# Kernel optimization log

Hardware: AMD Instinct MI355X
Metric: run time of the kernel (lower is better)

## Reference

```python
import jax, jax.numpy as jnp
import numpy as np

NUM_HEADS = 8
N_MOD = 3


def _sinusoidal_pe(seq_len, d_model):
    # standard sinusoidal table [seq_len, d_model]
    pos = np.arange(seq_len, dtype=np.float32)[:, None]
    div = np.exp(np.arange(0, d_model, 2, dtype=np.float32) * (-np.log(10000.0) / d_model))
    pe = np.zeros((seq_len, d_model), dtype=np.float32)
    pe[:, 0::2] = np.sin(pos * div)
    pe[:, 1::2] = np.cos(pos * div)
    return jnp.asarray(pe)


def _attn_mask(dim_x, dim_z, n_mod):
    # additive mask [dim_x, dim_x + n_mod*dim_z]: 0 where allowed, -inf elsewhere
    blocks = [np.eye(dim_x, dtype=np.float32)]
    for _ in range(n_mod):  # all modalities present (mod_list == full_mod)
        p2 = np.zeros((dim_x, dim_z), dtype=np.float32)
        p2[dim_x - dim_z:, :] = np.eye(dim_z, dtype=np.float32)
        blocks.append(p2)
    m = np.concatenate(blocks, axis=1)
    return jnp.asarray(np.where(m < 1, -np.inf, 0.0).astype(np.float32))


def setup_inputs() -> dict:
    key = jax.random.key(0)
    ks = jax.random.split(key, 8)
    bs, en, dx, dz = 32, 256, 512, 256
    state = jax.random.normal(ks[0], (bs, en, dx), jnp.float32)
    obs0 = jax.random.normal(ks[1], (bs, en, dz), jnp.float32)
    obs1 = jax.random.normal(ks[2], (bs, en, dz), jnp.float32)
    obs2 = jax.random.normal(ks[3], (bs, en, dz), jnp.float32)
    Q = jax.random.uniform(ks[4], (dx, en), jnp.float32)  # torch.rand init
    Wq = jax.random.normal(ks[5], (en, en), jnp.float32) / np.sqrt(en)
    Wk = jax.random.normal(ks[6], (en, en), jnp.float32) / np.sqrt(en)
    bq = jnp.zeros((en,), jnp.float32)
    bk = jnp.zeros((en,), jnp.float32)
    return {"state": state, "obs0": obs0, "obs1": obs1, "obs2": obs2,
            "Q": Q, "Wq": Wq, "bq": bq, "Wk": Wk, "bk": bk}


def reference(state, obs0, obs1, obs2, Q, Wq, bq, Wk, bk):
    bs, en, dx = state.shape
    dz = obs0.shape[2]
    obs_list = (obs0, obs1, obs2)
    mask = _attn_mask(dx, dz, N_MOD)            # [dx, L]
    pe = _sinusoidal_pe(bs, en)                 # positions run over batch axis (faithful quirk)

    # mean-center over the ensemble axis
    A = state - jnp.mean(state, axis=1, keepdims=True)          # [bs, en, dx]
    Ys = [o - jnp.mean(o, axis=1, keepdims=True) for o in obs_list]

    # build query / key-value sequences in [tokens, bs, en] layout, add PE, then batch-major
    q = Q[:, None, :] + pe[None, :, :]                          # [dx, bs, en]
    xy = jnp.concatenate([jnp.transpose(A, (2, 0, 1))]
                         + [jnp.transpose(Y, (2, 0, 1)) for Y in Ys], axis=0)
    xy = xy + pe[None, :, :]                                    # [L, bs, en]
    qb = jnp.transpose(q, (1, 0, 2))                            # [bs, dx, en]
    kb = jnp.transpose(xy, (1, 0, 2))                           # [bs, L, en]

    # multi-head masked attention (output path is discarded by the original module,
    # only the attention map is used, so no V/O projection is needed)
    dh = en // NUM_HEADS
    qh = (qb @ Wq + bq).reshape(bs, dx, NUM_HEADS, dh).transpose(0, 2, 1, 3)   # [bs,h,dx,dh]
    kh = (kb @ Wk + bk).reshape(bs, -1, NUM_HEADS, dh).transpose(0, 2, 1, 3)   # [bs,h,L,dh]
    scores = jnp.einsum('bhqd,bhkd->bhqk', qh, kh) / np.sqrt(dh).astype(np.float32)
    scores = scores + mask[None, None, :, :]
    atten = jnp.mean(jax.nn.softmax(scores, axis=-1), axis=1)   # [bs, dx, L]

    # attn-weighted matmul over concatenated raw state+obs
    merge = jnp.concatenate([state, obs0, obs1, obs2], axis=2)  # [bs, en, L]
    new_state = jnp.einsum('bql,bel->beq', atten, merge)        # [bs, en, dx]
    return new_state, atten
```

## Files before the change

### kernel.cpp

```cpp
#include <hip/hip_runtime.h>
#include <math.h>


__global__ __launch_bounds__(256)
void k_uv_copy(const float* __restrict__ Q, const float* __restrict__ Wq,
               const float* __restrict__ bq, const float* __restrict__ state,
               float* __restrict__ uT, float* __restrict__ vT,
               float* __restrict__ out0) {
  const int blk = blockIdx.x;
  const int t = threadIdx.x;
  if (blk < 288) {
    __shared__ float row[256];
    float rv;
    if (blk < 256) {
      rv = Q[(256 + blk) * 256 + t];
    } else {
      const int b = blk - 256;
      const float dv = expf(-9.210340371976184f * (float)((t >> 1) << 1) * (1.0f / 256.0f));
      const float ang = (float)b * dv;
      rv = (t & 1) ? cosf(ang) : sinf(ang);
    }
    row[t] = rv;
    __syncthreads();
    float acc = (blk < 256) ? 0.0f : bq[t];
    for (int e = 0; e < 256; ++e) acc += row[e] * Wq[e * 256 + t];
    if (blk < 256) uT[t * 256 + blk] = acc;
    else           vT[t * 32 + (blk - 256)] = acc;
  } else {
    const int id = blk - 288;
    const int b = id >> 5, eg = id & 31;
    const int r = t >> 5;
    const int c = t & 31;
    const int e = eg * 8 + r;
    const size_t base = ((size_t)(b * 256 + e)) * 512;
    *(float4*)(out0 + base + c * 4)        = *(const float4*)(state + base + c * 4);
    *(float4*)(out0 + base + (c + 32) * 4) = *(const float4*)(state + base + (c + 32) * 4);
  }
}

__global__ __launch_bounds__(256)
void k_w_onehot(const float* __restrict__ Wk, const float* __restrict__ uT,
                const float* __restrict__ vT, float* __restrict__ wu2,
                float* __restrict__ wv, float* __restrict__ out1) {
  const int blk = blockIdx.x;
  const int t = threadIdx.x;
  if (blk < 512) {
    const int e = blk & 255;
    const int part = blk >> 8;
    __shared__ float wrow[256];
    wrow[t] = Wk[e * 256 + t];
    __syncthreads();
    if (part == 0) {
#pragma unroll
      for (int h = 0; h < 8; ++h) {
        float acc = 0.0f;
#pragma unroll
        for (int d = 0; d < 32; ++d)
          acc += uT[(h * 32 + d) * 256 + t] * wrow[h * 32 + d];
        wu2[(h * 256 + e) * 256 + t] = acc;
      }
    } else if (t < 32) {
#pragma unroll
      for (int h = 0; h < 8; ++h) {
        float acc = 0.0f;
#pragma unroll
        for (int d = 0; d < 32; ++d)
          acc += vT[(h * 32 + d) * 32 + t] * wrow[h * 32 + d];
        wv[(t * 8 + h) * 256 + e] = acc;
      }
    }
  } else {
    const int id = blk - 512;
    const int b = id >> 5, qg = id & 31;
#pragma unroll
    for (int k = 0; k < 8; ++k) {
      const int q = qg * 8 + k;
      float4* row = (float4*)(out1 + ((size_t)(b * 512 + q)) * 1280);
      float4 o = make_float4(0.f, 0.f, 0.f, 0.f);
      if (t == (q >> 2)) {
        const int comp = q & 3;
        if (comp == 0) o.x = 1.f; else if (comp == 1) o.y = 1.f;
        else if (comp == 2) o.z = 1.f; else o.w = 1.f;
      }
      row[t] = o;
      if (t < 64) row[256 + t] = make_float4(0.f, 0.f, 0.f, 0.f);
    }
  }
}

__global__ __launch_bounds__(512)
void k_dot(const float* __restrict__ state, const float* __restrict__ o0,
           const float* __restrict__ o1, const float* __restrict__ o2,
           const float* __restrict__ wu2, const float* __restrict__ wv,
           float* __restrict__ pws) {
  const int t = threadIdx.x;
  const int jt = blockIdx.x;
  const int eq = blockIdx.y;
  const int b  = blockIdx.z;

  __shared__ float s_data[4][64][17];
  __shared__ float s_wv[512];
  __shared__ float s_part[8][16][25];

#pragma unroll
  for (int rep = 0; rep < 2; ++rep) {
    const int c = t + rep * 512;
    const int m = c >> 8;
    const int r = c & 255;
    const int e = r >> 2;
    const int jq = r & 3;
    const int ge = eq * 64 + e;
    const int j0 = jt * 16 + jq * 4;
    const float* src;
    if (m == 0)      src = state + ((size_t)(b * 256 + ge)) * 512 + 256 + j0;
    else if (m == 1) src = o0 + ((size_t)(b * 256 + ge)) * 256 + j0;
    else if (m == 2) src = o1 + ((size_t)(b * 256 + ge)) * 256 + j0;
    else             src = o2 + ((size_t)(b * 256 + ge)) * 256 + j0;
    const float4 v4 = *(const float4*)src;
    const int jb = jq * 4;
    s_data[m][e][jb]   = v4.x; s_data[m][e][jb+1] = v4.y;
    s_data[m][e][jb+2] = v4.z; s_data[m][e][jb+3] = v4.w;
  }
  s_wv[t & 511] = wv[b * 2048 + ((t & 511) >> 6) * 256 + eq * 64 + (t & 63)];
  __syncthreads();

  const int jl = t & 15;
  const int es = (t >> 4) & 15;
  const int hp = t >> 8;
  const int j = jt * 16 + jl;

  float acc[24];
#pragma unroll
  for (int k = 0; k < 24; ++k) acc[k] = 0.f;

  const float* pwu = wu2 + (size_t)hp * 4 * 256 * 256 + j;
  const float* pwv = s_wv + hp * 4 * 64;

#pragma unroll
  for (int it = 0; it < 4; ++it) {
    const int el = it * 16 + es;
    const int e = eq * 64 + el;
    const float s  = s_data[0][el][jl];
    const float x0 = s_data[1][el][jl];
    const float x1 = s_data[2][el][jl];
    const float x2 = s_data[3][el][jl];
    acc[20] += s; acc[21] += x0; acc[22] += x1; acc[23] += x2;
#pragma unroll
    for (int hh = 0; hh < 4; ++hh) {
      const float w = pwu[(size_t)(hh * 256 + e) * 256] + pwv[hh * 64 + el];
      acc[hh * 5 + 0] += s * w;  acc[hh * 5 + 1] += x0 * w;
      acc[hh * 5 + 2] += x1 * w; acc[hh * 5 + 3] += x2 * w;
      acc[hh * 5 + 4] += w;
    }
  }

#pragma unroll
  for (int k = 0; k < 24; ++k) {
    acc[k] += __shfl_xor(acc[k], 16);
    acc[k] += __shfl_xor(acc[k], 32);
  }
  if ((t & 48) == 0) {
    const int w = t >> 6;
    float* p = &s_part[w][jl][0];
#pragma unroll
    for (int k = 0; k < 24; ++k) p[k] = acc[k];
  }
  __syncthreads();

  const size_t base = (((size_t)(jt * 32 + b)) * 4 + eq) * 704;
  if (t < 16) {
#pragma unroll
    for (int k = 0; k < 20; ++k) {
      float s = s_part[0][t][k] + s_part[1][t][k] + s_part[2][t][k] + s_part[3][t][k];
      pws[base + k * 16 + t] = s;
    }
#pragma unroll
    for (int c = 0; c < 4; ++c) {
      float s = s_part[0][t][20 + c] + s_part[1][t][20 + c] +
                s_part[2][t][20 + c] + s_part[3][t][20 + c];
      pws[base + (40 + c) * 16 + t] = s;
    }
  } else if (t >= 256 && t < 272) {
    const int l = t & 15;
#pragma unroll
    for (int k = 0; k < 20; ++k) {
      float s = s_part[4][l][k] + s_part[5][l][k] + s_part[6][l][k] + s_part[7][l][k];
      pws[base + (20 + k) * 16 + l] = s;
    }
  }
}

__global__ __launch_bounds__(512)
void k_outA(const float* __restrict__ state, const float* __restrict__ o0,
            const float* __restrict__ o1, const float* __restrict__ o2,
            const float* __restrict__ pws, float* __restrict__ out0,
            float* __restrict__ out1) {
  const int blk = blockIdx.x;
  const int t = threadIdx.x;
  const int jt = blk & 15;
  const int b  = blk >> 4;
  __shared__ float s_tot[704];
  __shared__ float s_a[16][4];

  const size_t base = ((size_t)(jt * 32 + b)) * 2816;
  for (int i = t; i < 704; i += 512)
    s_tot[i] = (pws[base + i] + pws[base + 704 + i]) +
               (pws[base + 1408 + i] + pws[base + 2112 + i]);
  __syncthreads();

  if (t < 16) {
    float tot[44];
#pragma unroll
    for (int k = 0; k < 44; ++k) tot[k] = s_tot[k * 16 + t];
    const float m0 = tot[40] * (1.f / 256.f), m1 = tot[41] * (1.f / 256.f);
    const float m2 = tot[42] * (1.f / 256.f), m3 = tot[43] * (1.f / 256.f);
    const float inv = 0.17677669529663687f;
    float am0 = 0.f, am1 = 0.f, am2 = 0.f, am3 = 0.f;
#pragma unroll
    for (int h = 0; h < 8; ++h) {
      const float dO = tot[h * 5 + 4];
      const float s0 = (tot[h * 5 + 0] - m0 * dO) * inv;
      const float s1 = (tot[h * 5 + 1] - m1 * dO) * inv;
      const float s2 = (tot[h * 5 + 2] - m2 * dO) * inv;
      const float s3 = (tot[h * 5 + 3] - m3 * dO) * inv;
      const float mx = fmaxf(fmaxf(s0, s1), fmaxf(s2, s3));
      const float e0 = expf(s0 - mx), e1 = expf(s1 - mx);
      const float e2 = expf(s2 - mx), e3 = expf(s3 - mx);
      const float r = 1.f / (e0 + e1 + e2 + e3);
      am0 += e0 * r; am1 += e1 * r; am2 += e2 * r; am3 += e3 * r;
    }
    s_a[t][0] = am0 * 0.125f; s_a[t][1] = am1 * 0.125f;
    s_a[t][2] = am2 * 0.125f; s_a[t][3] = am3 * 0.125f;
  }
  __syncthreads();

  {
    const int jl2 = t & 15;
    const int er = t >> 4;
    const float a0 = s_a[jl2][0], a1 = s_a[jl2][1];
    const float a2 = s_a[jl2][2], a3 = s_a[jl2][3];
    const int jj = jt * 16 + jl2;
#pragma unroll
    for (int k = 0; k < 8; ++k) {
      const int e = er + 32 * k;
      const size_t idxS = ((size_t)(b * 256 + e)) * 512 + 256 + jj;
      const size_t idxO = ((size_t)(b * 256 + e)) * 256 + jj;
      out0[idxS] = a0 * state[idxS] + a1 * o0[idxO] + a2 * o1[idxO] + a3 * o2[idxO];
    }
  }

  {
    const int r = t >> 5;
    const int c = t & 31;
    const int j3 = jt * 16 + r;
    const int q = 256 + j3;
    const int comp = j3 & 3;
    const int tc0 = (256 + j3) >> 2, tc1 = (512 + j3) >> 2;
    const int tc2 = (768 + j3) >> 2, tc3 = (1024 + j3) >> 2;
    const float av0 = s_a[r][0], av1 = s_a[r][1];
    const float av2 = s_a[r][2], av3 = s_a[r][3];
    float4* orow = (float4*)(out1 + ((size_t)(b * 512 + q)) * 1280);
#pragma unroll
    for (int k = 0; k < 10; ++k) {
      const int c4 = c + 32 * k;
      float4 o = make_float4(0.f, 0.f, 0.f, 0.f);
      float val = 0.f; bool hit = false;
      if (c4 == tc0)      { val = av0; hit = true; }
      else if (c4 == tc1) { val = av1; hit = true; }
      else if (c4 == tc2) { val = av2; hit = true; }
      else if (c4 == tc3) { val = av3; hit = true; }
      if (hit) {
        if (comp == 0) o.x = val; else if (comp == 1) o.y = val;
        else if (comp == 2) o.z = val; else o.w = val;
      }
      orow[c4] = o;
    }
  }
}

extern "C" void kernel_launch(void* const* d_in, const int* in_sizes, int n_in,
                              void* d_out, int out_size, void* d_ws, size_t ws_size,
                              hipStream_t stream) {
  const float* state = (const float*)d_in[0];
  const float* obs0  = (const float*)d_in[1];
  const float* obs1  = (const float*)d_in[2];
  const float* obs2  = (const float*)d_in[3];
  const float* Q     = (const float*)d_in[4];
  const float* Wq    = (const float*)d_in[5];
  const float* bq    = (const float*)d_in[6];
  const float* Wk    = (const float*)d_in[7];

  float* out0 = (float*)d_out;
  float* out1 = out0 + (size_t)32 * 256 * 512;

  float* ws  = (float*)d_ws;
  float* uT  = ws;
  float* vT  = uT + 65536;
  float* wu2 = vT + 8192;
  float* wv  = wu2 + 524288;
  float* pws = wv + 65536;

  k_uv_copy<<<1312, 256, 0, stream>>>(Q, Wq, bq, state, uT, vT, out0);
  k_w_onehot<<<1536, 256, 0, stream>>>(Wk, uT, vT, wu2, wv, out1);
  k_dot<<<dim3(16, 4, 32), 512, 0, stream>>>(state, obs0, obs1, obs2, wu2, wv, pws);
  k_outA<<<512, 512, 0, stream>>>(state, obs0, obs1, obs2, pws, out0, out1);
}
```

Baseline: 67.28 us.

## Fuse dot-product and softmax/output kernels into one per-batch-tile kernel

Merges k_dot and k_outA into a single kernel. Each block now covers all 256 ensemble rows for one (jt, b) in two staged chunks, instead of splitting the ensemble axis across four blocks and reducing partial sums through global memory. This removes one kernel launch and the pws workspace round-trip. In exchange, the grid shrinks from 2048 to 512 blocks, each doing four times the work with more shared memory, so less parallelism is available to hide latency.

```diff
diff --git a/kernel.cpp b/kernel.cpp
--- a/kernel.cpp
+++ b/kernel.cpp
@@ -89,40 +89,21 @@
 }
 
 __global__ __launch_bounds__(512)
-void k_dot(const float* __restrict__ state, const float* __restrict__ o0,
+void k_all(const float* __restrict__ state, const float* __restrict__ o0,
            const float* __restrict__ o1, const float* __restrict__ o2,
            const float* __restrict__ wu2, const float* __restrict__ wv,
-           float* __restrict__ pws) {
+           float* __restrict__ out0, float* __restrict__ out1) {
   const int t = threadIdx.x;
   const int jt = blockIdx.x;
-  const int eq = blockIdx.y;
-  const int b  = blockIdx.z;
-
-  __shared__ float s_data[4][64][17];
-  __shared__ float s_wv[512];
+  const int b  = blockIdx.y;
+
+  __shared__ float s_data[4][128][17];
+  __shared__ float s_wvb[2048];
   __shared__ float s_part[8][16][25];
-
-#pragma unroll
-  for (int rep = 0; rep < 2; ++rep) {
-    const int c = t + rep * 512;
-    const int m = c >> 8;
-    const int r = c & 255;
-    const int e = r >> 2;
-    const int jq = r & 3;
-    const int ge = eq * 64 + e;
-    const int j0 = jt * 16 + jq * 4;
-    const float* src;
-    if (m == 0)      src = state + ((size_t)(b * 256 + ge)) * 512 + 256 + j0;
-    else if (m == 1) src = o0 + ((size_t)(b * 256 + ge)) * 256 + j0;
-    else if (m == 2) src = o1 + ((size_t)(b * 256 + ge)) * 256 + j0;
-    else             src = o2 + ((size_t)(b * 256 + ge)) * 256 + j0;
-    const float4 v4 = *(const float4*)src;
-    const int jb = jq * 4;
-    s_data[m][e][jb]   = v4.x; s_data[m][e][jb+1] = v4.y;
-    s_data[m][e][jb+2] = v4.z; s_data[m][e][jb+3] = v4.w;
-  }
-  s_wv[t & 511] = wv[b * 2048 + ((t & 511) >> 6) * 256 + eq * 64 + (t & 63)];
-  __syncthreads();
+  __shared__ float s_tot[44][16];
+  __shared__ float s_a[16][4];
+
+  for (int i = t; i < 2048; i += 512) s_wvb[i] = wv[b * 2048 + i];
 
   const int jl = t & 15;
   const int es = (t >> 4) & 15;
@@ -134,23 +115,48 @@
   for (int k = 0; k < 24; ++k) acc[k] = 0.f;
 
   const float* pwu = wu2 + (size_t)hp * 4 * 256 * 256 + j;
-  const float* pwv = s_wv + hp * 4 * 64;
-
-#pragma unroll
-  for (int it = 0; it < 4; ++it) {
-    const int el = it * 16 + es;
-    const int e = eq * 64 + el;
-    const float s  = s_data[0][el][jl];
-    const float x0 = s_data[1][el][jl];
-    const float x1 = s_data[2][el][jl];
-    const float x2 = s_data[3][el][jl];
-    acc[20] += s; acc[21] += x0; acc[22] += x1; acc[23] += x2;
-#pragma unroll
-    for (int hh = 0; hh < 4; ++hh) {
-      const float w = pwu[(size_t)(hh * 256 + e) * 256] + pwv[hh * 64 + el];
-      acc[hh * 5 + 0] += s * w;  acc[hh * 5 + 1] += x0 * w;
-      acc[hh * 5 + 2] += x1 * w; acc[hh * 5 + 3] += x2 * w;
-      acc[hh * 5 + 4] += w;
+  const float* pwvb = s_wvb + hp * 4 * 256;
+
+#pragma unroll
+  for (int chunk = 0; chunk < 2; ++chunk) {
+    __syncthreads();
+#pragma unroll
+    for (int rep = 0; rep < 4; ++rep) {
+      const int c = t + rep * 512;
+      const int m = c >> 9;
+      const int r = c & 511;
+      const int e = r >> 2;
+      const int jq = r & 3;
+      const int ge = chunk * 128 + e;
+      const int j0 = jt * 16 + jq * 4;
+      const float* src;
+      if (m == 0)      src = state + ((size_t)(b * 256 + ge)) * 512 + 256 + j0;
+      else if (m == 1) src = o0 + ((size_t)(b * 256 + ge)) * 256 + j0;
+      else if (m == 2) src = o1 + ((size_t)(b * 256 + ge)) * 256 + j0;
+      else             src = o2 + ((size_t)(b * 256 + ge)) * 256 + j0;
+      const float4 v4 = *(const float4*)src;
+      const int jb = jq * 4;
+      s_data[m][e][jb]   = v4.x; s_data[m][e][jb+1] = v4.y;
+      s_data[m][e][jb+2] = v4.z; s_data[m][e][jb+3] = v4.w;
+    }
+    __syncthreads();
+
+#pragma unroll
+    for (int it = 0; it < 8; ++it) {
+      const int el = it * 16 + es;
+      const int e = chunk * 128 + el;
+      const float s  = s_data[0][el][jl];
+      const float x0 = s_data[1][el][jl];
+      const float x1 = s_data[2][el][jl];
+      const float x2 = s_data[3][el][jl];
+      acc[20] += s; acc[21] += x0; acc[22] += x1; acc[23] += x2;
+#pragma unroll
+      for (int hh = 0; hh < 4; ++hh) {
+        const float w = pwu[(size_t)(hh * 256 + e) * 256] + pwvb[hh * 256 + e];
+        acc[hh * 5 + 0] += s * w;  acc[hh * 5 + 1] += x0 * w;
+        acc[hh * 5 + 2] += x1 * w; acc[hh * 5 + 3] += x2 * w;
+        acc[hh * 5 + 4] += w;
+      }
     }
   }
 
@@ -167,51 +173,26 @@
   }
   __syncthreads();
 
-  const size_t base = (((size_t)(jt * 32 + b)) * 4 + eq) * 704;
   if (t < 16) {
 #pragma unroll
-    for (int k = 0; k < 20; ++k) {
-      float s = s_part[0][t][k] + s_part[1][t][k] + s_part[2][t][k] + s_part[3][t][k];
-      pws[base + k * 16 + t] = s;
-    }
-#pragma unroll
-    for (int c = 0; c < 4; ++c) {
-      float s = s_part[0][t][20 + c] + s_part[1][t][20 + c] +
-                s_part[2][t][20 + c] + s_part[3][t][20 + c];
-      pws[base + (40 + c) * 16 + t] = s;
-    }
+    for (int k = 0; k < 20; ++k)
+      s_tot[k][t] = s_part[0][t][k] + s_part[1][t][k] + s_part[2][t][k] + s_part[3][t][k];
+#pragma unroll
+    for (int c = 0; c < 4; ++c)
+      s_tot[40 + c][t] = s_part[0][t][20 + c] + s_part[1][t][20 + c] +
+                         s_part[2][t][20 + c] + s_part[3][t][20 + c];
   } else if (t >= 256 && t < 272) {
     const int l = t & 15;
 #pragma unroll
-    for (int k = 0; k < 20; ++k) {
-      float s = s_part[4][l][k] + s_part[5][l][k] + s_part[6][l][k] + s_part[7][l][k];
-      pws[base + (20 + k) * 16 + l] = s;
-    }
-  }
-}
-
-__global__ __launch_bounds__(512)
-void k_outA(const float* __restrict__ state, const float* __restrict__ o0,
-            const float* __restrict__ o1, const float* __restrict__ o2,
-            const float* __restrict__ pws, float* __restrict__ out0,
-            float* __restrict__ out1) {
-  const int blk = blockIdx.x;
-  const int t = threadIdx.x;
-  const int jt = blk & 15;
-  const int b  = blk >> 4;
-  __shared__ float s_tot[704];
-  __shared__ float s_a[16][4];
-
-  const size_t base = ((size_t)(jt * 32 + b)) * 2816;
-  for (int i = t; i < 704; i += 512)
-    s_tot[i] = (pws[base + i] + pws[base + 704 + i]) +
-               (pws[base + 1408 + i] + pws[base + 2112 + i]);
+    for (int k = 0; k < 20; ++k)
+      s_tot[20 + k][l] = s_part[4][l][k] + s_part[5][l][k] + s_part[6][l][k] + s_part[7][l][k];
+  }
   __syncthreads();
 
   if (t < 16) {
     float tot[44];
 #pragma unroll
-    for (int k = 0; k < 44; ++k) tot[k] = s_tot[k * 16 + t];
+    for (int k = 0; k < 44; ++k) tot[k] = s_tot[k][t];
     const float m0 = tot[40] * (1.f / 256.f), m1 = tot[41] * (1.f / 256.f);
     const float m2 = tot[42] * (1.f / 256.f), m3 = tot[43] * (1.f / 256.f);
     const float inv = 0.17677669529663687f;
@@ -298,10 +279,8 @@
   float* vT  = uT + 65536;
   float* wu2 = vT + 8192;
   float* wv  = wu2 + 524288;
-  float* pws = wv + 65536;
 
   k_uv_copy<<<1312, 256, 0, stream>>>(Q, Wq, bq, state, uT, vT, out0);
   k_w_onehot<<<1536, 256, 0, stream>>>(Wk, uT, vT, wu2, wv, out1);
-  k_dot<<<dim3(16, 4, 32), 512, 0, stream>>>(state, obs0, obs1, obs2, wu2, wv, pws);
-  k_outA<<<512, 512, 0, stream>>>(state, obs0, obs1, obs2, pws, out0, out1);
-}
+  k_all<<<dim3(16, 32), 512, 0, stream>>>(state, obs0, obs1, obs2, wu2, wv, out0, out1);
+}
```

Result: faster. 63.89 us (-5.0%).
